# Optimization experiments

Hardware: AMD Instinct MI355X
Metric: run time of the kernel (lower is better)

## Reference

```python
import jax, jax.numpy as jnp
import numpy as np

# dims
A, T, K, H, NH, F, L = 64, 50, 6, 128, 8, 60, 512
M = A * T * K          # 19200 mode nodes (layout: agent, time, mode)
AT = A * T             # 3200 agent-timestep nodes
NL = 10                # GA layers: t2m,l2m,m2m_h,m2m_a,m2m_s,t2n,l2n,n2n_h,n2n_a,n2n_s
FF = 4 * H
E = 150000


def _ln(x, g, b):
    mu = x.mean(-1, keepdims=True)
    var = jnp.mean((x - mu) ** 2, axis=-1, keepdims=True)
    return (x - mu) * jax.lax.rsqrt(var + 1e-5) * g + b


def _mlp(x, W1, b1, W2, b2):
    return jax.nn.relu(x @ W1 + b1) @ W2 + b2


def _edge_emb(attr, i, eW1, eb1, eW2, eb2):
    # pad raw edge features to width 5 so all embed MLPs share a stacked param layout
    x = jnp.pad(attr, ((0, 0), (0, 5 - attr.shape[-1])))
    return jax.nn.relu(x @ eW1[i] + eb1[i]) @ eW2[i] + eb2[i]


def _segment_softmax(scores, dst, n):
    smax = jax.ops.segment_max(scores, dst, num_segments=n)
    smax = jnp.where(jnp.isfinite(smax), smax, 0.0)
    ex = jnp.exp(scores - smax[dst])
    den = jax.ops.segment_sum(ex, dst, num_segments=n)
    return ex / (den[dst] + 1e-9)


def _graph_attention(i, x_src, x_dst, ei, edge_emb, p):
    (Wq, Wk, Wv, Wo, Wke, Wve, g1, b1, g2, b2, fW1, fb1, fW2, fb2) = p
    src, dst = ei[0], ei[1]
    dh = H // NH
    n_dst = x_dst.shape[0]
    xd = _ln(x_dst, g1[i], b1[i])
    xs = _ln(x_src, g1[i], b1[i])
    q = (xd @ Wq[i]).reshape(n_dst, NH, dh)
    k = (xs @ Wk[i])[src]            # gather per-edge keys  [E,H]
    v = (xs @ Wv[i])[src]
    if edge_emb is not None:
        k = k + edge_emb @ Wke[i]
        v = v + edge_emb @ Wve[i]
    k = k.reshape(-1, NH, dh)
    v = v.reshape(-1, NH, dh)
    scores = jnp.sum(q[dst] * k, axis=-1) / np.sqrt(dh)   # [E,NH]
    attn = _segment_softmax(scores, dst, n_dst)
    agg = jax.ops.segment_sum(attn[..., None] * v, dst, num_segments=n_dst)
    x = x_dst + agg.reshape(n_dst, H) @ Wo[i]
    h = _ln(x, g2[i], b2[i])
    return x + _mlp(h, fW1[i], fb1[i], fW2[i], fb2[i])


def _forward(a_input, l_embs, mode_tokens,
             emb_W1, emb_b1, emb_W2, emb_b2,
             ga_Wq, ga_Wk, ga_Wv, ga_Wo, ga_Wke, ga_Wve,
             ga_g1, ga_b1, ga_g2, ga_b2, ga_fW1, ga_fb1, ga_fW2, ga_fb2,
             tp_W1, tp_b1, tp_W2, tp_b2,
             pa_W1, pa_b1, pa_W2, pa_b2,
             tr_W1, tr_b1, tr_W2, tr_b2,
             t2m_attr, l2m_attr, m2m_h_attr, m2m_a_attr,
             t2m_ei, l2m_ei, m2m_h_ei, m2m_a_ei, m2m_s_ei):
    ga = (ga_Wq, ga_Wk, ga_Wv, ga_Wo, ga_Wke, ga_Wve,
          ga_g1, ga_b1, ga_g2, ga_b2, ga_fW1, ga_fb1, ga_fW2, ga_fb2)
    # agent embedding: TwoLayerMLP on [vel_len, vel_theta, length, width, type]
    a_embs = (jax.nn.relu(a_input @ emb_W1[0] + emb_b1[0]) @ emb_W2[0] + emb_b2[0]).reshape(AT, H)
    # mode tokens broadcast over (agent, time)
    m = jnp.broadcast_to(mode_tokens, (A, T, K, H)).reshape(M, H)
    # edge-attr embeddings (gather-compute pattern)
    t2m_e = _edge_emb(t2m_attr, 1, emb_W1, emb_b1, emb_W2, emb_b2)
    l2m_e = _edge_emb(l2m_attr, 2, emb_W1, emb_b1, emb_W2, emb_b2)
    m2m_h_e = _edge_emb(m2m_h_attr, 3, emb_W1, emb_b1, emb_W2, emb_b2)
    m2m_a_e = _edge_emb(m2m_a_attr, 4, emb_W1, emb_b1, emb_W2, emb_b2)
    # proposal stage
    m = _graph_attention(0, a_embs, m, t2m_ei, t2m_e, ga)
    m = _graph_attention(1, l_embs, m, l2m_ei, l2m_e, ga)
    m = _graph_attention(2, m, m, m2m_h_ei, m2m_h_e, ga)
    m = _graph_attention(3, m, m, m2m_a_ei, m2m_a_e, ga)
    m = _graph_attention(4, m, m, m2m_s_ei, None, ga)
    m_last = m.reshape(A, T, K, H)[:, -1]                 # [A,K,H]
    proposal = _mlp(m_last, tp_W1, tp_b1, tp_W2, tp_b2)   # [A,K,2F]
    anchor = _mlp(proposal, pa_W1, pa_b1, pa_W2, pa_b2)   # [A,K,H]
    # refinement stage on anchor-conditioned mode nodes
    n = (m.reshape(A, T, K, H) + anchor[:, None]).reshape(M, H)
    n = _graph_attention(5, a_embs, n, t2m_ei, t2m_e, ga)
    n = _graph_attention(6, l_embs, n, l2m_ei, l2m_e, ga)
    n = _graph_attention(7, n, n, m2m_h_ei, m2m_h_e, ga)
    n = _graph_attention(8, n, n, m2m_a_ei, m2m_a_e, ga)
    n = _graph_attention(9, n, n, m2m_s_ei, None, ga)
    n_last = n.reshape(A, T, K, H)[:, -1]
    refine = proposal + _mlp(n_last, tr_W1, tr_b1, tr_W2, tr_b2)
    return jnp.stack([proposal, refine])                  # [2,A,K,2F]


def setup_inputs() -> dict:
    key = jax.random.key(0)
    ks = list(jax.random.split(key, 64))
    it = iter(ks)
    nx = lambda: next(it)
    p = lambda *s: 0.02 * jax.random.normal(nx(), s, dtype=jnp.float32)
    inp = {}
    inp['a_input'] = jax.random.normal(nx(), (A, T, 5), dtype=jnp.float32)
    inp['l_embs'] = jax.random.normal(nx(), (L, H), dtype=jnp.float32)
    inp['mode_tokens'] = p(K, H)
    # stacked edge/feature embed MLPs: 0:a,1:t2m,2:l2m,3:m2m_h,4:m2m_a
    inp['emb_W1'] = p(5, 5, H); inp['emb_b1'] = jnp.zeros((5, H), jnp.float32)
    inp['emb_W2'] = p(5, H, H); inp['emb_b2'] = jnp.zeros((5, H), jnp.float32)
    # stacked GraphAttention params
    for nm in ['ga_Wq', 'ga_Wk', 'ga_Wv', 'ga_Wo', 'ga_Wke', 'ga_Wve']:
        inp[nm] = p(NL, H, H)
    inp['ga_g1'] = jnp.ones((NL, H), jnp.float32); inp['ga_b1'] = jnp.zeros((NL, H), jnp.float32)
    inp['ga_g2'] = jnp.ones((NL, H), jnp.float32); inp['ga_b2'] = jnp.zeros((NL, H), jnp.float32)
    inp['ga_fW1'] = p(NL, H, FF); inp['ga_fb1'] = jnp.zeros((NL, FF), jnp.float32)
    inp['ga_fW2'] = p(NL, FF, H); inp['ga_fb2'] = jnp.zeros((NL, H), jnp.float32)
    # heads
    inp['tp_W1'] = p(H, H); inp['tp_b1'] = jnp.zeros((H,), jnp.float32)
    inp['tp_W2'] = p(H, 2 * F); inp['tp_b2'] = jnp.zeros((2 * F,), jnp.float32)
    inp['pa_W1'] = p(2 * F, H); inp['pa_b1'] = jnp.zeros((H,), jnp.float32)
    inp['pa_W2'] = p(H, H); inp['pa_b2'] = jnp.zeros((H,), jnp.float32)
    inp['tr_W1'] = p(H, H); inp['tr_b1'] = jnp.zeros((H,), jnp.float32)
    inp['tr_W2'] = p(H, 2 * F); inp['tr_b2'] = jnp.zeros((2 * F,), jnp.float32)
    # raw edge features
    inp['t2m_attr'] = jax.random.normal(nx(), (E, 4), dtype=jnp.float32)
    inp['l2m_attr'] = jax.random.normal(nx(), (E, 3), dtype=jnp.float32)
    inp['m2m_h_attr'] = jax.random.normal(nx(), (E, 4), dtype=jnp.float32)
    inp['m2m_a_attr'] = jax.random.normal(nx(), (E, 3), dtype=jnp.float32)
    # edge indices (src row range differs per graph)
    ri = lambda hi: jax.random.randint(nx(), (E,), 0, hi, dtype=jnp.int32)
    inp['t2m_ei'] = jnp.stack([ri(AT), ri(M)])
    inp['l2m_ei'] = jnp.stack([ri(L), ri(M)])
    inp['m2m_h_ei'] = jnp.stack([ri(M), ri(M)])
    inp['m2m_a_ei'] = jnp.stack([ri(M), ri(M)])
    inp['m2m_s_ei'] = jnp.stack([ri(M), ri(M)])
    return inp


def reference(a_input, l_embs, mode_tokens,
              emb_W1, emb_b1, emb_W2, emb_b2,
              ga_Wq, ga_Wk, ga_Wv, ga_Wo, ga_Wke, ga_Wve,
              ga_g1, ga_b1, ga_g2, ga_b2, ga_fW1, ga_fb1, ga_fW2, ga_fb2,
              tp_W1, tp_b1, tp_W2, tp_b2,
              pa_W1, pa_b1, pa_W2, pa_b2,
              tr_W1, tr_b1, tr_W2, tr_b2,
              t2m_attr, l2m_attr, m2m_h_attr, m2m_a_attr,
              t2m_ei, l2m_ei, m2m_h_ei, m2m_a_ei, m2m_s_ei):
    return _forward(a_input, l_embs, mode_tokens,
                    emb_W1, emb_b1, emb_W2, emb_b2,
                    ga_Wq, ga_Wk, ga_Wv, ga_Wo, ga_Wke, ga_Wve,
                    ga_g1, ga_b1, ga_g2, ga_b2, ga_fW1, ga_fb1, ga_fW2, ga_fb2,
                    tp_W1, tp_b1, tp_W2, tp_b2,
                    pa_W1, pa_b1, pa_W2, pa_b2,
                    tr_W1, tr_b1, tr_W2, tr_b2,
                    t2m_attr, l2m_attr, m2m_h_attr, m2m_a_attr,
                    t2m_ei, l2m_ei, m2m_h_ei, m2m_a_ei, m2m_s_ei)
```

## Files before the change

### kernel.cpp

```cpp
#include <hip/hip_runtime.h>
#include <hip/hip_bf16.h>
#include <math.h>

#define DEV __device__ __forceinline__

typedef __attribute__((ext_vector_type(4))) float floatx4;
typedef __attribute__((ext_vector_type(8))) __bf16 bf16x8;

static constexpr int A_ = 64, T_ = 50, K_ = 6, H_ = 128, NH_ = 8, F_ = 60, L_ = 512;
static constexpr int M_  = A_ * T_ * K_;
static constexpr int AT_ = A_ * T_;
static constexpr int FF_ = 4 * H_;
static constexpr int NL_ = 10;
static constexpr int P2F = 2 * F_;
static constexpr int AK_ = A_ * K_;
static constexpr size_t WLAY = 196608;
static constexpr int NB_ = (M_ + 255) / 256;

DEV ushort f2bh(float f) {
    unsigned u = __float_as_uint(f);
    unsigned r = u + 0x7FFFu + ((u >> 16) & 1u);
    return (ushort)(r >> 16);
}
DEV float bh2f(ushort h) { return __uint_as_float(((unsigned)h) << 16); }

__global__ __launch_bounds__(256) void ln_stats(const float* __restrict__ x,
                                                float* __restrict__ mu,
                                                float* __restrict__ rs, int n) {
    int row = blockIdx.x * 4 + (threadIdx.x >> 6);
    int lane = threadIdx.x & 63;
    if (row >= n) return;
    const float* xr = x + (size_t)row * H_;
    float v0 = xr[lane], v1 = xr[lane + 64];
    float s = v0 + v1;
    for (int m = 32; m >= 1; m >>= 1) s += __shfl_xor(s, m, 64);
    float m_ = s * (1.f / 128.f);
    float d0 = v0 - m_, d1 = v1 - m_;
    float vs = d0 * d0 + d1 * d1;
    for (int m = 32; m >= 1; m >>= 1) vs += __shfl_xor(vs, m, 64);
    if (lane == 0) {
        mu[row] = m_;
        rs[row] = rsqrtf(vs * (1.f / 128.f) + 1e-5f);
    }
}

template <int ACT, bool RES, int OMODE, bool LNX>
__global__ __launch_bounds__(256) void mgemm(const float* __restrict__ X,
                                             const ushort* __restrict__ Wh,
                                             const ushort* __restrict__ Wl,
                                             const float* __restrict__ bias,
                                             const float* __restrict__ res,
                                             float* __restrict__ Y,
                                             ushort* __restrict__ Yb,
                                             const float* __restrict__ muv,
                                             const float* __restrict__ rsv,
                                             const float* __restrict__ lng,
                                             const float* __restrict__ lnb,
                                             int n, int Kd, int C) {
    __shared__ ushort lds[4 * 8192];
    ushort* Xh  = lds;
    ushort* Xl  = lds + 8192;
    ushort* Wsh = lds + 16384;
    ushort* Wsl = lds + 24576;
    int row0 = blockIdx.x * 128, col0 = blockIdx.y * 128;
    int tid = threadIdx.x;
    int lane = tid & 63, wid = tid >> 6;
    int rbase = (wid >> 1) * 64, cbase = (wid & 1) * 64;
    int lrow = lane & 15, lk = lane >> 4;
    floatx4 acc[4][4];
#pragma unroll
    for (int a = 0; a < 4; a++)
#pragma unroll
        for (int b2 = 0; b2 < 4; b2++) acc[a][b2] = floatx4{0.f, 0.f, 0.f, 0.f};

    for (int k0 = 0; k0 < Kd; k0 += 64) {
        float4 g4, b4;
        if (LNX) {
            int kcol = k0 + (tid & 15) * 4;
            g4 = *(const float4*)(lng + kcol);
            b4 = *(const float4*)(lnb + kcol);
        }
#pragma unroll
        for (int i = 0; i < 8; i++) {
            int idx = tid + i * 256;
            int r = idx >> 4, kc = idx & 15;
            float4 v = *(const float4*)(X + (size_t)(row0 + r) * Kd + k0 + kc * 4);
            if (LNX) {
                float mur = muv[row0 + r];
                float rsr = rsv[row0 + r];
                v.x = (v.x - mur) * rsr * g4.x + b4.x;
                v.y = (v.y - mur) * rsr * g4.y + b4.y;
                v.z = (v.z - mur) * rsr * g4.z + b4.z;
                v.w = (v.w - mur) * rsr * g4.w + b4.w;
            }
            ushort h0 = f2bh(v.x), h1 = f2bh(v.y), h2 = f2bh(v.z), h3 = f2bh(v.w);
            ushort l0 = f2bh(v.x - bh2f(h0)), l1 = f2bh(v.y - bh2f(h1)),
                   l2 = f2bh(v.z - bh2f(h2)), l3 = f2bh(v.w - bh2f(h3));
            int base = (r << 6) + (((kc >> 1) ^ (r & 7)) << 3) + ((kc & 1) << 2);
            *(ushort4*)(Xh + base) = make_ushort4(h0, h1, h2, h3);
            *(ushort4*)(Xl + base) = make_ushort4(l0, l1, l2, l3);
        }
#pragma unroll
        for (int i = 0; i < 4; i++) {
            int idx = tid + i * 256;
            int c = idx >> 3, ch = idx & 7;
            int base = (c << 6) + ((ch ^ (c & 7)) << 3);
            size_t go = (size_t)(col0 + c) * Kd + k0 + ch * 8;
            *(float4*)(Wsh + base) = *(const float4*)(Wh + go);
            *(float4*)(Wsl + base) = *(const float4*)(Wl + go);
        }
        __syncthreads();
#pragma unroll
        for (int kk = 0; kk < 2; kk++) {
            int ch = kk * 4 + lk;
            bf16x8 xh[4], xl[4], wh[4], wl[4];
#pragma unroll
            for (int s = 0; s < 4; s++) {
                int r = rbase + s * 16 + lrow;
                int xoff = (r << 6) + ((ch ^ (r & 7)) << 3);
                xh[s] = *(const bf16x8*)(Xh + xoff);
                xl[s] = *(const bf16x8*)(Xl + xoff);
                int c = cbase + s * 16 + lrow;
                int woff = (c << 6) + ((ch ^ (c & 7)) << 3);
                wh[s] = *(const bf16x8*)(Wsh + woff);
                wl[s] = *(const bf16x8*)(Wsl + woff);
            }
#pragma unroll
            for (int sr = 0; sr < 4; sr++)
#pragma unroll
                for (int sc = 0; sc < 4; sc++) {
                    acc[sr][sc] = __builtin_amdgcn_mfma_f32_16x16x32_bf16(wh[sc], xh[sr], acc[sr][sc], 0, 0, 0);
                    acc[sr][sc] = __builtin_amdgcn_mfma_f32_16x16x32_bf16(wl[sc], xh[sr], acc[sr][sc], 0, 0, 0);
                    acc[sr][sc] = __builtin_amdgcn_mfma_f32_16x16x32_bf16(wh[sc], xl[sr], acc[sr][sc], 0, 0, 0);
                }
        }
        __syncthreads();
    }
#pragma unroll
    for (int sr = 0; sr < 4; sr++) {
        int row = row0 + rbase + sr * 16 + lrow;
#pragma unroll
        for (int sc = 0; sc < 4; sc++) {
            int col = col0 + cbase + sc * 16 + lk * 4;
            float4 v = make_float4(acc[sr][sc][0], acc[sr][sc][1],
                                   acc[sr][sc][2], acc[sr][sc][3]);
            if (bias) { float4 bv = *(const float4*)(bias + col);
                        v.x += bv.x; v.y += bv.y; v.z += bv.z; v.w += bv.w; }
            if (ACT == 1) { v.x = fmaxf(v.x, 0.f); v.y = fmaxf(v.y, 0.f);
                            v.z = fmaxf(v.z, 0.f); v.w = fmaxf(v.w, 0.f); }
            if (OMODE == 0) {
                size_t o = (size_t)row * C + col;
                if (RES) { float4 rv = *(const float4*)(res + o);
                           v.x += rv.x; v.y += rv.y; v.z += rv.z; v.w += rv.w; }
                *(float4*)(Y + o) = v;
            } else if (OMODE == 1) {
                size_t o = (size_t)row * C + col;
                *(ushort4*)(Yb + o) = make_ushort4(f2bh(v.x), f2bh(v.y), f2bh(v.z), f2bh(v.w));
            } else {
                if (col0 == 0) {
                    *(float4*)(Y + (size_t)row * 128 + col) = v;
                } else {
                    *(ushort4*)(Yb + (size_t)row * 256 + (col - 128)) =
                        make_ushort4(f2bh(v.x), f2bh(v.y), f2bh(v.z), f2bh(v.w));
                }
            }
        }
    }
}

__global__ __launch_bounds__(256) void prep_w(const float* __restrict__ Wq,
                                              const float* __restrict__ Wk,
                                              const float* __restrict__ Wv,
                                              const float* __restrict__ Wo,
                                              const float* __restrict__ fW1,
                                              const float* __restrict__ fW2,
                                              ushort* __restrict__ oh,
                                              ushort* __restrict__ ol) {
    int l = blockIdx.y, t = blockIdx.x;
    const float* src; int K, C, tiles_c; size_t obase;
    if (t < 64) {
        int mi = t >> 4; t &= 15;
        src = (mi == 0 ? Wq : mi == 1 ? Wk : mi == 2 ? Wv : Wo) + (size_t)l * 16384;
        K = 128; C = 128; tiles_c = 4; obase = (size_t)l * WLAY + (size_t)mi * 16384;
    } else if (t < 128) {
        t -= 64; src = fW1 + (size_t)l * 65536;
        K = 128; C = 512; tiles_c = 16; obase = (size_t)l * WLAY + 65536;
    } else {
        t -= 128; src = fW2 + (size_t)l * 65536;
        K = 512; C = 128; tiles_c = 4; obase = (size_t)l * WLAY + 131072;
    }
    int tc = t % tiles_c, tk = t / tiles_c;
    __shared__ float tile[32][33];
    int tx = threadIdx.x & 31, ty = threadIdx.x >> 5;
#pragma unroll
    for (int i = 0; i < 4; i++) {
        int k = tk * 32 + ty + i * 8;
        tile[ty + i * 8][tx] = src[(size_t)k * C + tc * 32 + tx];
    }
    __syncthreads();
#pragma unroll
    for (int i = 0; i < 4; i++) {
        int c = tc * 32 + ty + i * 8;
        float v = tile[tx][ty + i * 8];
        ushort h = f2bh(v);
        ushort lo = f2bh(v - bh2f(h));
        size_t o = obase + (size_t)c * K + tk * 32 + tx;
        oh[o] = h; ol[o] = lo;
    }
}

template <int ACT, bool RES>
__global__ void small_gemm(const float* __restrict__ X, const float* __restrict__ W,
                           const float* __restrict__ bias, const float* __restrict__ res,
                           float* __restrict__ Y, int n, int Kd, int C) {
    int idx = blockIdx.x * 256 + threadIdx.x;
    if (idx >= n * C) return;
    int row = idx / C, c = idx - row * C;
    float a = bias ? bias[c] : 0.f;
    const float* xr = X + (size_t)row * Kd;
    for (int k = 0; k < Kd; k++) a = fmaf(xr[k], W[(size_t)k * C + c], a);
    if (ACT == 1) a = fmaxf(a, 0.f);
    if (RES) a += res[idx];
    Y[idx] = a;
}

__global__ __launch_bounds__(256) void combine_fast(const float* __restrict__ eW2,
                                                    const float* __restrict__ Wke,
                                                    const float* __restrict__ Wve,
                                                    float* __restrict__ cW) {
    __shared__ float Xs[128 * 36];
    __shared__ float Ws[32 * 128];
    int x = blockIdx.x;
    int li = x & 7, kv = x >> 3;
    int l = li < 4 ? li : li + 1;
    int g = (li & 3) + 1;
    const float* E2 = eW2 + (size_t)g * 16384;
    const float* Wp = (kv ? Wve : Wke) + (size_t)l * 16384;
    float* out = cW + (size_t)l * 32768 + kv * 128;
    int tid = threadIdx.x;
    int tc = tid & 15, tr = tid >> 4;
    int cA = tc * 4, rA = tr * 4;
    float acc[8][8] = {};
    for (int j0 = 0; j0 < 128; j0 += 32) {
#pragma unroll
        for (int i = 0; i < 4; i++) {
            int idx = tid + i * 256;
            int r = idx >> 3, jc = idx & 7;
            *(float4*)(Xs + r * 36 + jc * 4) =
                *(const float4*)(E2 + (size_t)r * 128 + j0 + jc * 4);
        }
#pragma unroll
        for (int i = 0; i < 4; i++) {
            int idx = tid + i * 256;
            int cc = idx & 31, jj = idx >> 5;
            *(float4*)(Ws + jj * 128 + cc * 4) =
                *(const float4*)(Wp + (size_t)(j0 + jj) * 128 + cc * 4);
        }
        __syncthreads();
#pragma unroll 8
        for (int jj = 0; jj < 32; jj++) {
            float4 w0 = *(const float4*)(Ws + jj * 128 + cA);
            float4 w1 = *(const float4*)(Ws + jj * 128 + cA + 64);
            float xr[8];
#pragma unroll
            for (int i2 = 0; i2 < 4; i2++) {
                xr[i2]     = Xs[(rA + i2) * 36 + jj];
                xr[4 + i2] = Xs[(rA + i2 + 64) * 36 + jj];
            }
#pragma unroll
            for (int i2 = 0; i2 < 8; i2++) {
                float xv = xr[i2];
                acc[i2][0] = fmaf(xv, w0.x, acc[i2][0]);
                acc[i2][1] = fmaf(xv, w0.y, acc[i2][1]);
                acc[i2][2] = fmaf(xv, w0.z, acc[i2][2]);
                acc[i2][3] = fmaf(xv, w0.w, acc[i2][3]);
                acc[i2][4] = fmaf(xv, w1.x, acc[i2][4]);
                acc[i2][5] = fmaf(xv, w1.y, acc[i2][5]);
                acc[i2][6] = fmaf(xv, w1.z, acc[i2][6]);
                acc[i2][7] = fmaf(xv, w1.w, acc[i2][7]);
            }
        }
        __syncthreads();
    }
#pragma unroll
    for (int i = 0; i < 8; i++) {
        int r = (i < 4) ? (rA + i) : (rA + i + 60);
#pragma unroll
        for (int chh = 0; chh < 2; chh++) {
            int c = cA + chh * 64;
            *(float4*)(out + (size_t)r * 256 + c) =
                make_float4(acc[i][chh * 4 + 0], acc[i][chh * 4 + 1],
                            acc[i][chh * 4 + 2], acc[i][chh * 4 + 3]);
        }
    }
}
__global__ void combine_bias(const float* __restrict__ eb2,
                             const float* __restrict__ Wke,
                             const float* __restrict__ Wve,
                             float* __restrict__ cb) {
    int x = blockIdx.x;
    int li = x & 7, kv = x >> 3;
    int l = li < 4 ? li : li + 1;
    int g = (li & 3) + 1;
    const float* Wp = (kv ? Wve : Wke) + (size_t)l * 16384;
    const float* eb = eb2 + g * 128;
    int cc = threadIdx.x;
    float a = 0.f;
    for (int j = 0; j < 128; j++) a = fmaf(eb[j], Wp[(size_t)j * 128 + cc], a);
    cb[l * 256 + kv * 128 + cc] = a;
}

__global__ void zero_i32(int* __restrict__ p, int n) {
    int i = blockIdx.x * 256 + threadIdx.x;
    if (i < n) p[i] = 0;
}
__global__ void hist_kernel(const int* __restrict__ dst, int E, int* __restrict__ deg) {
    int e = blockIdx.x * 256 + threadIdx.x;
    if (e < E) atomicAdd(&deg[dst[e]], 1);
}
__global__ __launch_bounds__(256) void exscan5(const int* __restrict__ deg0,
                                               int* __restrict__ off0,
                                               int* __restrict__ cursor0, int n) {
    int g = blockIdx.x;
    const int* deg = deg0 + (size_t)g * n;
    int* off = off0 + (size_t)g * (n + 1);
    int* cursor = cursor0 + (size_t)g * n;
    __shared__ int wsum[4];
    __shared__ int carry;
    int tid = threadIdx.x, lane = tid & 63, w = tid >> 6;
    if (tid == 0) carry = 0;
    __syncthreads();
    for (int base = 0; base < n; base += 256) {
        int v = (base + tid < n) ? deg[base + tid] : 0;
        int incl = v;
        for (int d = 1; d < 64; d <<= 1) {
            int t = __shfl_up(incl, d, 64);
            if (lane >= d) incl += t;
        }
        if (lane == 63) wsum[w] = incl;
        __syncthreads();
        int woff = 0;
        for (int i = 0; i < w; i++) woff += wsum[i];
        int total = wsum[0] + wsum[1] + wsum[2] + wsum[3];
        int excl = carry + woff + incl - v;
        if (base + tid < n) { off[base + tid] = excl; cursor[base + tid] = excl; }
        __syncthreads();
        if (tid == 0) carry += total;
        __syncthreads();
    }
    if (threadIdx.x == 0) off[n] = carry;
}
__global__ void scatter_kernel(const int* __restrict__ dst, int E,
                               int* __restrict__ cursor, int* __restrict__ eids) {
    int e = blockIdx.x * 256 + threadIdx.x;
    if (e < E) { int p = atomicAdd(&cursor[dst[e]], 1); eids[p] = e; }
}
__global__ void sort_edges(const int* __restrict__ eid, const int* __restrict__ srcArr,
                           const float* __restrict__ attr, int aw, int E,
                           int* __restrict__ esrc, float4* __restrict__ eattr) {
    int pos = blockIdx.x * 256 + threadIdx.x;
    if (pos >= E) return;
    int e = eid[pos];
    esrc[pos] = srcArr[e];
    if (attr) {
        float4 v;
        v.x = attr[(size_t)e * aw + 0];
        v.y = attr[(size_t)e * aw + 1];
        v.z = (aw > 2) ? attr[(size_t)e * aw + 2] : 0.f;
        v.w = (aw > 3) ? attr[(size_t)e * aw + 3] : 0.f;
        eattr[pos] = v;
    }
}

__global__ __launch_bounds__(256) void hist_deg2(const int* __restrict__ deg5, int n,
                                                 int* __restrict__ bh) {
    int g = blockIdx.y;
    const int* deg = deg5 + (size_t)g * n;
    __shared__ int lh[33];
    if (threadIdx.x < 33) lh[threadIdx.x] = 0;
    __syncthreads();
    int d = blockIdx.x * 256 + threadIdx.x;
    if (d < n) { int b = deg[d]; if (b > 32) b = 32; atomicAdd(&lh[b], 1); }
    __syncthreads();
    if (threadIdx.x < 33)
        bh[((size_t)g * NB_ + blockIdx.x) * 33 + threadIdx.x] = lh[threadIdx.x];
}
__global__ __launch_bounds__(64) void scan_bh(int* __restrict__ bh) {
    int g = blockIdx.x;
    int* p = bh + (size_t)g * NB_ * 33;
    __shared__ int tot[33], base[33];
    int bin = threadIdx.x;
    if (bin < 33) {
        int t = 0;
        for (int b = 0; b < NB_; b++) t += p[b * 33 + bin];
        tot[bin] = t;
    }
    __syncthreads();
    if (threadIdx.x == 0) {
        int acc = 0;
        for (int i = 0; i < 33; i++) { base[i] = acc; acc += tot[i]; }
    }
    __syncthreads();
    if (bin < 33) {
        int run = base[bin];
        for (int b = 0; b < NB_; b++) { int v = p[b * 33 + bin]; p[b * 33 + bin] = run; run += v; }
    }
}
__global__ __launch_bounds__(256) void scatter_ord2(const int* __restrict__ deg5, int n,
                                                    const int* __restrict__ bh,
                                                    int* __restrict__ dord5) {
    int g = blockIdx.y;
    const int* deg = deg5 + (size_t)g * n;
    int* dord = dord5 + (size_t)g * n;
    __shared__ int cur[33];
    if (threadIdx.x < 33)
        cur[threadIdx.x] = bh[((size_t)g * NB_ + blockIdx.x) * 33 + threadIdx.x];
    __syncthreads();
    int d = blockIdx.x * 256 + threadIdx.x;
    if (d < n) {
        int b = deg[d]; if (b > 32) b = 32;
        int p = atomicAdd(&cur[b], 1);
        dord[p] = d;
    }
}

__global__ __launch_bounds__(256) void prep_g(const float* __restrict__ q,
                                              const float* __restrict__ cWl,
                                              const float* __restrict__ cbl,
                                              ushort* __restrict__ g,
                                              float* __restrict__ sb) {
    __shared__ float qs[8 * 132];
    int tid = threadIdx.x;
    int cp = tid & 127, hb = (tid >> 7) * 4;
    float ck[64];
    {
        const float* csrc = cWl + (size_t)cp * 256 + hb * 16;
#pragma unroll
        for (int t4 = 0; t4 < 16; t4++) {
            float4 v = *(const float4*)(csrc + t4 * 4);
            ck[t4 * 4 + 0] = v.x; ck[t4 * 4 + 1] = v.y;
            ck[t4 * 4 + 2] = v.z; ck[t4 * 4 + 3] = v.w;
        }
    }
    int d0 = blockIdx.x * 8;
    {
        int dl = tid >> 5, col = (tid & 31) * 4;
        *(float4*)(qs + dl * 132 + col) = *(const float4*)(q + (size_t)(d0 + dl) * 128 + col);
    }
    __syncthreads();
#pragma unroll
    for (int dl = 0; dl < 8; dl++) {
        const float* qr = qs + dl * 132 + hb * 16;
        float a0 = 0.f, a1 = 0.f, a2 = 0.f, a3 = 0.f;
#pragma unroll
        for (int t = 0; t < 16; t++) {
            a0 = fmaf(ck[t],      qr[t],      a0);
            a1 = fmaf(ck[16 + t], qr[16 + t], a1);
            a2 = fmaf(ck[32 + t], qr[32 + t], a2);
            a3 = fmaf(ck[48 + t], qr[48 + t], a3);
        }
        ushort4 o = make_ushort4(f2bh(a0 * 0.25f), f2bh(a1 * 0.25f),
                                 f2bh(a2 * 0.25f), f2bh(a3 * 0.25f));
        *(ushort4*)(g + (size_t)(d0 + dl) * 1024 + cp * 8 + hb) = o;
    }
    if (tid < 64) {
        int dl = tid >> 3, h = tid & 7;
        const float* qr = qs + dl * 132 + h * 16;
        const float* cbr = cbl + h * 16;
        float a = 0.f;
#pragma unroll
        for (int t = 0; t < 16; t++) a = fmaf(cbr[t], qr[t], a);
        sb[(d0 + dl) * 8 + h] = a * 0.25f;
    }
}

__global__ __launch_bounds__(256) void attn_fact(const int* __restrict__ dord,
                                                 const int* __restrict__ off,
                                                 const int* __restrict__ esrc,
                                                 const float4* __restrict__ eattr,
                                                 const ushort* __restrict__ g,
                                                 const float* __restrict__ sb,
                                                 const float* __restrict__ eW1,
                                                 const float* __restrict__ eb1,
                                                 const float* __restrict__ q,
                                                 const ushort* __restrict__ kvp,
                                                 ushort* __restrict__ hsum,
                                                 float* __restrict__ vxacc,
                                                 float* __restrict__ den) {
    __shared__ float lds[4 * 144];
    int w = threadIdx.x >> 6, l = threadIdx.x & 63;
    int i = l & 15, hlo = l >> 4;
    float* hw = lds + w * 144;
    int d = dord[blockIdx.x * 4 + w];
    int beg = off[d], end = off[d + 1];
    float q0 = q[(size_t)d * 128 + l] * 0.25f;
    float q1 = q[(size_t)d * 128 + 64 + l] * 0.25f;
    float gA[8], gB[8];
#pragma unroll
    for (int j = 0; j < 8; j++) {
        gA[j] = bh2f(g[(size_t)d * 1024 + (j * 16 + i) * 8 + hlo]);
        gB[j] = bh2f(g[(size_t)d * 1024 + (j * 16 + i) * 8 + hlo + 4]);
    }
    float sbA = sb[d * 8 + hlo], sbB = sb[d * 8 + 4 + hlo];
    float w1a[4], w1b[4];
#pragma unroll
    for (int j = 0; j < 4; j++) { w1a[j] = eW1[j * 128 + l]; w1b[j] = eW1[j * 128 + 64 + l]; }
    float ebA = eb1[l], ebB = eb1[64 + l];
    float dnA = 0.f, dnB = 0.f;
    float accL[8] = {}, accH[8] = {};
    float va0 = 0.f, va1 = 0.f;
    float4 atA = make_float4(0.f, 0.f, 0.f, 0.f), atB = atA;
    ushort kA0 = 0, kA1 = 0, vA0 = 0, vA1 = 0;
    ushort kB0 = 0, kB1 = 0, vB0 = 0, vB1 = 0;
    auto LOADE = [&](int p, float4& at, ushort& ka, ushort& kb, ushort& va, ushort& vb) {
        int s = esrc[p]; at = eattr[p];
        const ushort* r = kvp + (size_t)s * 256;
        ka = r[l]; kb = r[64 + l];
        va = r[128 + l]; vb = r[192 + l];
    };
    if (beg < end) LOADE(beg, atA, kA0, kA1, vA0, vA1);
    if (beg + 1 < end) LOADE(beg + 1, atB, kB0, kB1, vB0, vB1);
    for (int pos = beg; pos < end; pos++) {
        float4 at = atA;
        ushort rk0 = kA0, rk1 = kA1, rv0 = vA0, rv1 = vA1;
        atA = atB; kA0 = kB0; kA1 = kB1; vA0 = vB0; vA1 = vB1;
        if (pos + 2 < end) LOADE(pos + 2, atB, kB0, kB1, vB0, vB1);
        float h0 = fmaxf(ebA + at.x * w1a[0] + at.y * w1a[1] + at.z * w1a[2] + at.w * w1a[3], 0.f);
        float h1 = fmaxf(ebB + at.x * w1b[0] + at.y * w1b[1] + at.z * w1b[2] + at.w * w1b[3], 0.f);
        hw[l] = h0; hw[64 + l] = h1;
        __builtin_amdgcn_wave_barrier();
        float pA = q0 * bh2f(rk0), pB = q1 * bh2f(rk1);
#pragma unroll
        for (int j = 0; j < 8; j++) {
            float hv = hw[j * 16 + i];
            pA = fmaf(hv, gA[j], pA);
            pB = fmaf(hv, gB[j], pB);
        }
#pragma unroll
        for (int msk = 1; msk < 16; msk <<= 1) {
            pA += __shfl_xor(pA, msk, 64);
            pB += __shfl_xor(pB, msk, 64);
        }
        float wA = __expf(pA + sbA);
        float wB = __expf(pB + sbB);
        dnA += wA; dnB += wB;
        va0 = fmaf(wA, bh2f(rv0), va0);
        va1 = fmaf(wB, bh2f(rv1), va1);
        if (i == 0) { hw[128 + hlo] = wA; hw[132 + hlo] = wB; }
        __builtin_amdgcn_wave_barrier();
        float4 WA = *(float4*)(hw + 128), WB = *(float4*)(hw + 132);
#pragma unroll
        for (int j = 0; j < 4; j++) {
            float wa = ((const float*)&WA)[j];
            float wb = ((const float*)&WB)[j];
            accL[j]     = fmaf(wa, h0, accL[j]);
            accH[j]     = fmaf(wa, h1, accH[j]);
            accL[4 + j] = fmaf(wb, h0, accL[4 + j]);
            accH[4 + j] = fmaf(wb, h1, accH[4 + j]);
        }
    }
#pragma unroll
    for (int h = 0; h < 8; h++) {
        hsum[(size_t)d * 1024 + h * 128 + l]      = f2bh(accL[h]);
        hsum[(size_t)d * 1024 + h * 128 + 64 + l] = f2bh(accH[h]);
    }
    vxacc[(size_t)d * 128 + l] = va0;
    vxacc[(size_t)d * 128 + 64 + l] = va1;
    if (i == 0) { den[d * 8 + hlo] = dnA; den[d * 8 + 4 + hlo] = dnB; }
}

__global__ __launch_bounds__(256) void attn_plain(const int* __restrict__ dord,
                                                  const int* __restrict__ off,
                                                  const int* __restrict__ esrc,
                                                  const float* __restrict__ q,
                                                  const ushort* __restrict__ kvp,
                                                  float* __restrict__ agg) {
    int lane = threadIdx.x & 63;
    int d = dord[blockIdx.x * 4 + (threadIdx.x >> 6)];
    int beg = off[d], end = off[d + 1];
    float q0 = q[(size_t)d * 128 + lane] * 0.25f;
    float q1 = q[(size_t)d * 128 + 64 + lane] * 0.25f;
    float den0 = 0.f, den1 = 0.f, acc0 = 0.f, acc1 = 0.f;
    ushort kA0 = 0, kA1 = 0, vA0 = 0, vA1 = 0;
    ushort kB0 = 0, kB1 = 0, vB0 = 0, vB1 = 0;
    auto LOADE = [&](int p, ushort& ka, ushort& kb, ushort& va, ushort& vb) {
        int s = esrc[p];
        const ushort* r = kvp + (size_t)s * 256;
        ka = r[lane]; kb = r[64 + lane];
        va = r[128 + lane]; vb = r[192 + lane];
    };
    if (beg < end) LOADE(beg, kA0, kA1, vA0, vA1);
    if (beg + 1 < end) LOADE(beg + 1, kB0, kB1, vB0, vB1);
    for (int pos = beg; pos < end; pos++) {
        ushort rk0 = kA0, rk1 = kA1, rv0 = vA0, rv1 = vA1;
        kA0 = kB0; kA1 = kB1; vA0 = vB0; vA1 = vB1;
        if (pos + 2 < end) LOADE(pos + 2, kB0, kB1, vB0, vB1);
        float p0 = q0 * bh2f(rk0), p1 = q1 * bh2f(rk1);
#pragma unroll
        for (int msk = 1; msk < 16; msk <<= 1) {
            p0 += __shfl_xor(p0, msk, 64);
            p1 += __shfl_xor(p1, msk, 64);
        }
        float w0 = __expf(p0), w1 = __expf(p1);
        den0 += w0; den1 += w1;
        acc0 = fmaf(w0, bh2f(rv0), acc0);
        acc1 = fmaf(w1, bh2f(rv1), acc1);
    }
    agg[(size_t)d * 128 + lane]      = acc0 / (den0 + 1e-9f);
    agg[(size_t)d * 128 + 64 + lane] = acc1 / (den1 + 1e-9f);
}

static constexpr int HST_ = 1092;
__global__ __launch_bounds__(256) void agg_fin(const ushort* __restrict__ hsum,
                                               const float* __restrict__ vxacc,
                                               const float* __restrict__ den,
                                               const float* __restrict__ cWl,
                                               const float* __restrict__ cbl,
                                               float* __restrict__ agg) {
    __shared__ float Cvs[128 * 128];
    __shared__ float hstage[8 * HST_];
    __shared__ float dens[64];
    int tid = threadIdx.x;
    {
        int cp = tid >> 1, cb0 = (tid & 1) * 64;
#pragma unroll
        for (int kq = 0; kq < 16; kq++)
            *(float4*)(Cvs + cp * 128 + cb0 + kq * 4) =
                *(const float4*)(cWl + (size_t)cp * 256 + 128 + cb0 + kq * 4);
    }
    int j = tid & 31, dsel = tid >> 5;
    int c4 = j * 4, h = j >> 2;
    float4 cvb = *(const float4*)(cbl + 128 + c4);
    for (int d0 = blockIdx.x * 8; d0 < M_; d0 += gridDim.x * 8) {
        __syncthreads();
        int r = tid * 4;
#pragma unroll
        for (int k = 0; k < 8; k++) {
            ushort4 u = *(const ushort4*)(hsum + (size_t)(d0 + k) * 1024 + r);
            *(float4*)(hstage + k * HST_ + (r >> 7) * 136 + (r & 127)) =
                make_float4(bh2f(u.x), bh2f(u.y), bh2f(u.z), bh2f(u.w));
        }
        if (tid < 64) dens[tid] = den[d0 * 8 + tid];
        __syncthreads();
        int d = d0 + dsel;
        float dn = dens[dsel * 8 + h];
        float inv = 1.f / (dn + 1e-9f);
        float cf = dn * inv;
        float a0 = 0.f, a1 = 0.f, a2 = 0.f, a3 = 0.f;
        const float* hrow = hstage + dsel * HST_ + h * 136;
#pragma unroll 4
        for (int cpp = 0; cpp < 128; cpp++) {
            float hs = hrow[cpp];
            float4 cv = *(float4*)(Cvs + cpp * 128 + c4);
            a0 = fmaf(hs, cv.x, a0); a1 = fmaf(hs, cv.y, a1);
            a2 = fmaf(hs, cv.z, a2); a3 = fmaf(hs, cv.w, a3);
        }
        float4 vv = *(const float4*)(vxacc + (size_t)d * 128 + c4);
        float4 o;
        o.x = (vv.x + a0) * inv + cvb.x * cf;
        o.y = (vv.y + a1) * inv + cvb.y * cf;
        o.z = (vv.z + a2) * inv + cvb.z * cf;
        o.w = (vv.w + a3) * inv + cvb.w * cf;
        *(float4*)(agg + (size_t)d * 128 + c4) = o;
    }
}

__global__ void mode_init(float* __restrict__ m, const float* __restrict__ mt) {
    int idx = blockIdx.x * 256 + threadIdx.x;
    if (idx >= M_ * H_) return;
    int node = idx >> 7, c = idx & 127;
    m[idx] = mt[(node % K_) * H_ + c];
}
__global__ void extract_last(const float* __restrict__ m, float* __restrict__ out) {
    int idx = blockIdx.x * 256 + threadIdx.x;
    if (idx >= AK_ * H_) return;
    int row = idx >> 7, c = idx & 127;
    int a = row / K_, k = row - a * K_;
    int node = (a * T_ + (T_ - 1)) * K_ + k;
    out[idx] = m[(size_t)node * H_ + c];
}
__global__ void add_anchor(float* __restrict__ m, const float* __restrict__ anchor) {
    int idx = blockIdx.x * 256 + threadIdx.x;
    if (idx >= M_ * H_) return;
    int node = idx >> 7, c = idx & 127;
    int a = node / (T_ * K_), k = node % K_;
    m[idx] += anchor[(size_t)(a * K_ + k) * H_ + c];
}

extern "C" void kernel_launch(void* const* d_in, const int* in_sizes, int n_in,
                              void* d_out, int out_size, void* d_ws, size_t ws_size,
                              hipStream_t stream) {
    const float* a_input     = (const float*)d_in[0];
    const float* l_embs      = (const float*)d_in[1];
    const float* mode_tokens = (const float*)d_in[2];
    const float* emb_W1 = (const float*)d_in[3];
    const float* emb_b1 = (const float*)d_in[4];
    const float* emb_W2 = (const float*)d_in[5];
    const float* emb_b2 = (const float*)d_in[6];
    const float* ga_Wq  = (const float*)d_in[7];
    const float* ga_Wk  = (const float*)d_in[8];
    const float* ga_Wv  = (const float*)d_in[9];
    const float* ga_Wo  = (const float*)d_in[10];
    const float* ga_Wke = (const float*)d_in[11];
    const float* ga_Wve = (const float*)d_in[12];
    const float* ga_g1  = (const float*)d_in[13];
    const float* ga_b1  = (const float*)d_in[14];
    const float* ga_g2  = (const float*)d_in[15];
    const float* ga_b2  = (const float*)d_in[16];
    const float* ga_fW1 = (const float*)d_in[17];
    const float* ga_fb1 = (const float*)d_in[18];
    const float* ga_fW2 = (const float*)d_in[19];
    const float* ga_fb2 = (const float*)d_in[20];
    const float* tp_W1 = (const float*)d_in[21];
    const float* tp_b1 = (const float*)d_in[22];
    const float* tp_W2 = (const float*)d_in[23];
    const float* tp_b2 = (const float*)d_in[24];
    const float* pa_W1 = (const float*)d_in[25];
    const float* pa_b1 = (const float*)d_in[26];
    const float* pa_W2 = (const float*)d_in[27];
    const float* pa_b2 = (const float*)d_in[28];
    const float* tr_W1 = (const float*)d_in[29];
    const float* tr_b1 = (const float*)d_in[30];
    const float* tr_W2 = (const float*)d_in[31];
    const float* tr_b2 = (const float*)d_in[32];
    const float* attrs[4] = { (const float*)d_in[33], (const float*)d_in[34],
                              (const float*)d_in[35], (const float*)d_in[36] };
    const int* eis[5] = { (const int*)d_in[37], (const int*)d_in[38], (const int*)d_in[39],
                          (const int*)d_in[40], (const int*)d_in[41] };
    int Es[5];
    int Emax = 0;
    for (int i = 0; i < 5; i++) { Es[i] = in_sizes[37 + i] / 2; if (Es[i] > Emax) Emax = Es[i]; }

    size_t off = 0;
    auto alloc = [&](size_t nbytes) -> char* {
        char* p = (char*)d_ws + off;
        off += ((nbytes + 255) / 256) * 256;
        return p;
    };
    float* cW     = (float*)alloc((size_t)NL_ * 128 * 256 * 4);
    float* cb     = (float*)alloc((size_t)NL_ * 256 * 4);
    ushort* wbh   = (ushort*)alloc((size_t)NL_ * WLAY * 2);
    ushort* wbl   = (ushort*)alloc((size_t)NL_ * WLAY * 2);
    float* a_embs = (float*)alloc((size_t)AT_ * H_ * 4);
    float* m      = (float*)alloc((size_t)M_ * H_ * 4);
    float* q      = (float*)alloc((size_t)M_ * H_ * 4);
    ushort* kvb   = (ushort*)alloc((size_t)M_ * 256 * 2);
    float* agg    = (float*)alloc((size_t)M_ * H_ * 4);
    float* big    = (float*)alloc((size_t)M_ * FF_ * 4);
    ushort* gbuf  = (ushort*)alloc((size_t)M_ * 1024 * 2);
    ushort* hsumb = (ushort*)alloc((size_t)M_ * 1024 * 2);
    float* vxacc  = (float*)alloc((size_t)M_ * H_ * 4);
    float* den    = (float*)alloc((size_t)M_ * 8 * 4);
    float* sb     = (float*)alloc((size_t)M_ * 8 * 4);
    float* muM    = (float*)alloc((size_t)M_ * 4);
    float* rsM    = (float*)alloc((size_t)M_ * 4);
    float* muA    = (float*)alloc((size_t)AT_ * 4);
    float* rsA    = (float*)alloc((size_t)AT_ * 4);
    float* muL    = (float*)alloc((size_t)L_ * 4);
    float* rsL    = (float*)alloc((size_t)L_ * 4);
    int* csr_off  = (int*)alloc((size_t)5 * (M_ + 1) * 4);
    int* csr_eid  = (int*)alloc((size_t)5 * Emax * 4);
    int* esrc     = (int*)alloc((size_t)5 * Emax * 4);
    float4* eattr = (float4*)alloc((size_t)4 * Emax * 16);
    int* deg5     = (int*)alloc((size_t)5 * M_ * 4);
    int* cursor5  = (int*)alloc((size_t)5 * M_ * 4);
    int* dord5    = (int*)alloc((size_t)5 * M_ * 4);
    int* bh5      = (int*)alloc((size_t)5 * NB_ * 33 * 4);
    float* mlast  = (float*)alloc((size_t)AK_ * H_ * 4);
    float* hbuf   = (float*)alloc((size_t)AK_ * H_ * 4);
    float* anchor = (float*)alloc((size_t)AK_ * H_ * 4);
    (void)ws_size; (void)n_in;

    float* outp = (float*)d_out;

    zero_i32<<<(5 * M_ + 255) / 256, 256, 0, stream>>>(deg5, 5 * M_);
    for (int gI = 0; gI < 5; gI++)
        hist_kernel<<<(Es[gI] + 255) / 256, 256, 0, stream>>>(eis[gI] + Es[gI], Es[gI], deg5 + (size_t)gI * M_);
    exscan5<<<5, 256, 0, stream>>>(deg5, csr_off, cursor5, M_);
    for (int gI = 0; gI < 5; gI++)
        scatter_kernel<<<(Es[gI] + 255) / 256, 256, 0, stream>>>(eis[gI] + Es[gI], Es[gI],
            cursor5 + (size_t)gI * M_, csr_eid + (size_t)gI * Emax);
    for (int gI = 0; gI < 5; gI++) {
        int aw = (gI == 0 || gI == 2) ? 4 : (gI == 4 ? 0 : 3);
        sort_edges<<<(Es[gI] + 255) / 256, 256, 0, stream>>>(
            csr_eid + (size_t)gI * Emax, eis[gI], (gI < 4) ? attrs[gI] : nullptr, aw, Es[gI],
            esrc + (size_t)gI * Emax, eattr + (size_t)gI * Emax);
    }
    hist_deg2<<<dim3(NB_, 5), 256, 0, stream>>>(deg5, M_, bh5);
    scan_bh<<<5, 64, 0, stream>>>(bh5);
    scatter_ord2<<<dim3(NB_, 5), 256, 0, stream>>>(deg5, M_, bh5, dord5);

    prep_w<<<dim3(192, 10), 256, 0, stream>>>(ga_Wq, ga_Wk, ga_Wv, ga_Wo, ga_fW1, ga_fW2, wbh, wbl);
    combine_fast<<<16, 256, 0, stream>>>(emb_W2, ga_Wke, ga_Wve, cW);
    combine_bias<<<16, 128, 0, stream>>>(emb_b2, ga_Wke, ga_Wve, cb);

    small_gemm<1, false><<<(AT_ * H_ + 255) / 256, 256, 0, stream>>>(a_input, emb_W1, emb_b1, nullptr, big, AT_, 5, H_);
    small_gemm<0, false><<<(AT_ * H_ + 255) / 256, 256, 0, stream>>>(big, emb_W2, emb_b2, nullptr, a_embs, AT_, H_, H_);
    mode_init<<<(M_ * H_ + 255) / 256, 256, 0, stream>>>(m, mode_tokens);
    ln_stats<<<AT_ / 4, 256, 0, stream>>>(a_embs, muA, rsA, AT_);
    ln_stats<<<L_ / 4, 256, 0, stream>>>(l_embs, muL, rsL, L_);

    struct Cfg { const float* srcX; const float* muS; const float* rsS; int n_src; int gi; bool hasE; };
    Cfg cfgs[10] = {
        { a_embs, muA, rsA, AT_, 0, true }, { l_embs, muL, rsL, L_, 1, true },
        { nullptr, nullptr, nullptr, M_, 2, true }, { nullptr, nullptr, nullptr, M_, 3, true },
        { nullptr, nullptr, nullptr, M_, 4, false },
        { a_embs, muA, rsA, AT_, 0, true }, { l_embs, muL, rsL, L_, 1, true },
        { nullptr, nullptr, nullptr, M_, 2, true }, { nullptr, nullptr, nullptr, M_, 3, true },
        { nullptr, nullptr, nullptr, M_, 4, false },
    };

    for (int l = 0; l < 10; l++) {
        const Cfg& cf = cfgs[l];
        const int* offg = csr_off + cf.gi * (M_ + 1);
        const int* esrcg = esrc + (size_t)cf.gi * Emax;
        const float4* eattrg = eattr + (size_t)cf.gi * Emax;
        const int* dordg = dord5 + (size_t)cf.gi * M_;
        const float* g1 = ga_g1 + l * H_; const float* b1 = ga_b1 + l * H_;
        size_t wb = (size_t)l * WLAY;

        ln_stats<<<M_ / 4, 256, 0, stream>>>(m, muM, rsM, M_);
        if (cf.srcX) {
            mgemm<0, false, 0, true><<<dim3(M_ / 128, 1), 256, 0, stream>>>(
                m, wbh + wb, wbl + wb, nullptr, nullptr, q, nullptr,
                muM, rsM, g1, b1, M_, 128, 128);
            mgemm<0, false, 1, true><<<dim3(cf.n_src / 128, 2), 256, 0, stream>>>(
                cf.srcX, wbh + wb + 16384, wbl + wb + 16384, nullptr, nullptr, nullptr, kvb,
                cf.muS, cf.rsS, g1, b1, cf.n_src, 128, 256);
        } else {
            mgemm<0, false, 2, true><<<dim3(M_ / 128, 3), 256, 0, stream>>>(
                m, wbh + wb, wbl + wb, nullptr, nullptr, q, kvb,
                muM, rsM, g1, b1, M_, 128, 384);
        }

        if (cf.hasE) {
            int gg = (l < 5) ? l + 1 : l - 4;
            const float* eW1g = emb_W1 + (size_t)gg * 5 * H_;
            const float* eb1g = emb_b1 + (size_t)gg * H_;
            prep_g<<<M_ / 8, 256, 0, stream>>>(q, cW + (size_t)l * 128 * 256, cb + l * 256, gbuf, sb);
            attn_fact<<<M_ / 4, 256, 0, stream>>>(dordg, offg, esrcg, eattrg, gbuf, sb, eW1g, eb1g,
                                                  q, kvb, hsumb, vxacc, den);
            agg_fin<<<256, 256, 0, stream>>>(hsumb, vxacc, den,
                                             cW + (size_t)l * 128 * 256, cb + l * 256, agg);
        } else {
            attn_plain<<<M_ / 4, 256, 0, stream>>>(dordg, offg, esrcg, q, kvb, agg);
        }

        mgemm<0, true, 0, false><<<dim3(M_ / 128, 1), 256, 0, stream>>>(
            agg, wbh + wb + 49152, wbl + wb + 49152, nullptr, m, m, nullptr,
            nullptr, nullptr, nullptr, nullptr, M_, 128, 128);
        ln_stats<<<M_ / 4, 256, 0, stream>>>(m, muM, rsM, M_);
        mgemm<1, false, 0, true><<<dim3(M_ / 128, 4), 256, 0, stream>>>(
            m, wbh + wb + 65536, wbl + wb + 65536, ga_fb1 + l * FF_, nullptr, big, nullptr,
            muM, rsM, ga_g2 + l * H_, ga_b2 + l * H_, M_, 128, 512);
        mgemm<0, true, 0, false><<<dim3(M_ / 128, 1), 256, 0, stream>>>(
            big, wbh + wb + 131072, wbl + wb + 131072, ga_fb2 + l * H_, m, m, nullptr,
            nullptr, nullptr, nullptr, nullptr, M_, 512, 128);

        if (l == 4) {
            extract_last<<<(AK_ * H_ + 255) / 256, 256, 0, stream>>>(m, mlast);
            small_gemm<1, false><<<(AK_ * H_ + 255) / 256, 256, 0, stream>>>(mlast, tp_W1, tp_b1, nullptr, hbuf, AK_, H_, H_);
            small_gemm<0, false><<<(AK_ * P2F + 255) / 256, 256, 0, stream>>>(hbuf, tp_W2, tp_b2, nullptr, outp, AK_, H_, P2F);
            small_gemm<1, false><<<(AK_ * H_ + 255) / 256, 256, 0, stream>>>(outp, pa_W1, pa_b1, nullptr, hbuf, AK_, P2F, H_);
            small_gemm<0, false><<<(AK_ * H_ + 255) / 256, 256, 0, stream>>>(hbuf, pa_W2, pa_b2, nullptr, anchor, AK_, H_, H_);
            add_anchor<<<(M_ * H_ + 255) / 256, 256, 0, stream>>>(m, anchor);
        }
    }

    extract_last<<<(AK_ * H_ + 255) / 256, 256, 0, stream>>>(m, mlast);
    small_gemm<1, false><<<(AK_ * H_ + 255) / 256, 256, 0, stream>>>(mlast, tr_W1, tr_b1, nullptr, hbuf, AK_, H_, H_);
    small_gemm<0, true><<<(AK_ * P2F + 255) / 256, 256, 0, stream>>>(hbuf, tr_W2, tr_b2, outp, outp + AK_ * P2F, AK_, H_, P2F);
}
```

Baseline: 2.654 ms.

## Fuse LayerNorm stats into residual GEMM epilogues and merge agg_fin into attn_fact

The residual-output GEMMs now compute per-row sum and sum of squares in their epilogue and write mean and rstd directly. This removes the standalone ln_stats passes before each attention block and before the FFN; ln_stats still runs at init and after the anchor add. The agg_fin kernel is folded into attn_fact, which stages per-destination results in shared memory and applies the value projection in-block. That avoids writing and rereading the bf16 hsum, vxacc and den buffers. The trade-offs are a one-pass variance formula (E[x²]−μ²) that is less numerically stable, and a per-block fp32 matvec that reads cW from global memory instead of shared memory.

```diff
diff --git a/kernel.cpp b/kernel.cpp
--- a/kernel.cpp
+++ b/kernel.cpp
@@ -44,7 +44,7 @@
     }
 }
 
-template <int ACT, bool RES, int OMODE, bool LNX>
+template <int ACT, bool RES, int OMODE, bool LNX, bool STATS>
 __global__ __launch_bounds__(256) void mgemm(const float* __restrict__ X,
                                              const ushort* __restrict__ Wh,
                                              const ushort* __restrict__ Wl,
@@ -56,6 +56,8 @@
                                              const float* __restrict__ rsv,
                                              const float* __restrict__ lng,
                                              const float* __restrict__ lnb,
+                                             float* __restrict__ muo,
+                                             float* __restrict__ rso,
                                              int n, int Kd, int C) {
     __shared__ ushort lds[4 * 8192];
     ushort* Xh  = lds;
@@ -136,6 +138,7 @@
         }
         __syncthreads();
     }
+    float rowsum[4] = {}, rowsq[4] = {};
 #pragma unroll
     for (int sr = 0; sr < 4; sr++) {
         int row = row0 + rbase + sr * 16 + lrow;
@@ -152,6 +155,10 @@
                 size_t o = (size_t)row * C + col;
                 if (RES) { float4 rv = *(const float4*)(res + o);
                            v.x += rv.x; v.y += rv.y; v.z += rv.z; v.w += rv.w; }
+                if (STATS) {
+                    rowsum[sr] += v.x + v.y + v.z + v.w;
+                    rowsq[sr]  += v.x * v.x + v.y * v.y + v.z * v.z + v.w * v.w;
+                }
                 *(float4*)(Y + o) = v;
             } else if (OMODE == 1) {
                 size_t o = (size_t)row * C + col;
@@ -164,6 +171,27 @@
                         make_ushort4(f2bh(v.x), f2bh(v.y), f2bh(v.z), f2bh(v.w));
                 }
             }
+        }
+    }
+    if (STATS) {
+        float* sums = (float*)lds;
+        float* sqs  = ((float*)lds) + 1024;
+        int slot = (wid & 1) * 4 + lk;
+#pragma unroll
+        for (int sr = 0; sr < 4; sr++) {
+            int rl = rbase + sr * 16 + lrow;
+            sums[rl * 8 + slot] = rowsum[sr];
+            sqs[rl * 8 + slot]  = rowsq[sr];
+        }
+        __syncthreads();
+        if (tid < 128) {
+            float s = 0.f, sq = 0.f;
+#pragma unroll
+            for (int t = 0; t < 8; t++) { s += sums[tid * 8 + t]; sq += sqs[tid * 8 + t]; }
+            float mu = s * (1.f / 128.f);
+            float var = sq * (1.f / 128.f) - mu * mu;
+            muo[row0 + tid] = mu;
+            rso[row0 + tid] = rsqrtf(var + 1e-5f);
         }
     }
 }
@@ -484,13 +512,17 @@
                                                  const float* __restrict__ eb1,
                                                  const float* __restrict__ q,
                                                  const ushort* __restrict__ kvp,
-                                                 ushort* __restrict__ hsum,
-                                                 float* __restrict__ vxacc,
-                                                 float* __restrict__ den) {
-    __shared__ float lds[4 * 144];
+                                                 const float* __restrict__ cWl,
+                                                 const float* __restrict__ cbl,
+                                                 float* __restrict__ agg) {
+    __shared__ float hw4[4 * 144];
+    __shared__ float hstage[4][1024];
+    __shared__ float vstage[4][128];
+    __shared__ float dens2[4][8];
+    __shared__ int sD[4];
     int w = threadIdx.x >> 6, l = threadIdx.x & 63;
     int i = l & 15, hlo = l >> 4;
-    float* hw = lds + w * 144;
+    float* hw = hw4 + w * 144;
     int d = dord[blockIdx.x * 4 + w];
     int beg = off[d], end = off[d + 1];
     float q0 = q[(size_t)d * 128 + l] * 0.25f;
@@ -561,12 +593,35 @@
     }
 #pragma unroll
     for (int h = 0; h < 8; h++) {
-        hsum[(size_t)d * 1024 + h * 128 + l]      = f2bh(accL[h]);
-        hsum[(size_t)d * 1024 + h * 128 + 64 + l] = f2bh(accH[h]);
-    }
-    vxacc[(size_t)d * 128 + l] = va0;
-    vxacc[(size_t)d * 128 + 64 + l] = va1;
-    if (i == 0) { den[d * 8 + hlo] = dnA; den[d * 8 + 4 + hlo] = dnB; }
+        hstage[w][h * 128 + l]      = accL[h];
+        hstage[w][h * 128 + 64 + l] = accH[h];
+    }
+    vstage[w][l] = va0; vstage[w][64 + l] = va1;
+    if (i == 0) { dens2[w][hlo] = dnA; dens2[w][4 + hlo] = dnB; }
+    if (l == 0) sD[w] = d;
+    __syncthreads();
+    {
+        int cc = threadIdx.x & 127, grp = threadIdx.x >> 7;
+        int ds0 = grp * 2, ds1 = grp * 2 + 1;
+        int hh = cc >> 4;
+        float dn0 = dens2[ds0][hh], dn1 = dens2[ds1][hh];
+        float inv0 = 1.f / (dn0 + 1e-9f), cf0 = dn0 * inv0;
+        float inv1 = 1.f / (dn1 + 1e-9f), cf1 = dn1 * inv1;
+        const float* hr0 = &hstage[ds0][hh * 128];
+        const float* hr1 = &hstage[ds1][hh * 128];
+        const float* cvp = cWl + 128 + cc;
+        float a0 = 0.f, a1 = 0.f;
+#pragma unroll 4
+        for (int cp = 0; cp < 128; cp++) {
+            float cv = cvp[(size_t)cp * 256];
+            a0 = fmaf(hr0[cp], cv, a0);
+            a1 = fmaf(hr1[cp], cv, a1);
+        }
+        float cvb = cbl[128 + cc];
+        int dd0 = sD[ds0], dd1 = sD[ds1];
+        agg[(size_t)dd0 * 128 + cc] = (vstage[ds0][cc] + a0) * inv0 + cvb * cf0;
+        agg[(size_t)dd1 * 128 + cc] = (vstage[ds1][cc] + a1) * inv1 + cvb * cf1;
+    }
 }
 
 __global__ __launch_bounds__(256) void attn_plain(const int* __restrict__ dord,
@@ -608,61 +663,6 @@
     }
     agg[(size_t)d * 128 + lane]      = acc0 / (den0 + 1e-9f);
     agg[(size_t)d * 128 + 64 + lane] = acc1 / (den1 + 1e-9f);
-}
-
-static constexpr int HST_ = 1092;
-__global__ __launch_bounds__(256) void agg_fin(const ushort* __restrict__ hsum,
-                                               const float* __restrict__ vxacc,
-                                               const float* __restrict__ den,
-                                               const float* __restrict__ cWl,
-                                               const float* __restrict__ cbl,
-                                               float* __restrict__ agg) {
-    __shared__ float Cvs[128 * 128];
-    __shared__ float hstage[8 * HST_];
-    __shared__ float dens[64];
-    int tid = threadIdx.x;
-    {
-        int cp = tid >> 1, cb0 = (tid & 1) * 64;
-#pragma unroll
-        for (int kq = 0; kq < 16; kq++)
-            *(float4*)(Cvs + cp * 128 + cb0 + kq * 4) =
-                *(const float4*)(cWl + (size_t)cp * 256 + 128 + cb0 + kq * 4);
-    }
-    int j = tid & 31, dsel = tid >> 5;
-    int c4 = j * 4, h = j >> 2;
-    float4 cvb = *(const float4*)(cbl + 128 + c4);
-    for (int d0 = blockIdx.x * 8; d0 < M_; d0 += gridDim.x * 8) {
-        __syncthreads();
-        int r = tid * 4;
-#pragma unroll
-        for (int k = 0; k < 8; k++) {
-            ushort4 u = *(const ushort4*)(hsum + (size_t)(d0 + k) * 1024 + r);
-            *(float4*)(hstage + k * HST_ + (r >> 7) * 136 + (r & 127)) =
-                make_float4(bh2f(u.x), bh2f(u.y), bh2f(u.z), bh2f(u.w));
-        }
-        if (tid < 64) dens[tid] = den[d0 * 8 + tid];
-        __syncthreads();
-        int d = d0 + dsel;
-        float dn = dens[dsel * 8 + h];
-        float inv = 1.f / (dn + 1e-9f);
-        float cf = dn * inv;
-        float a0 = 0.f, a1 = 0.f, a2 = 0.f, a3 = 0.f;
-        const float* hrow = hstage + dsel * HST_ + h * 136;
-#pragma unroll 4
-        for (int cpp = 0; cpp < 128; cpp++) {
-            float hs = hrow[cpp];
-            float4 cv = *(float4*)(Cvs + cpp * 128 + c4);
-            a0 = fmaf(hs, cv.x, a0); a1 = fmaf(hs, cv.y, a1);
-            a2 = fmaf(hs, cv.z, a2); a3 = fmaf(hs, cv.w, a3);
-        }
-        float4 vv = *(const float4*)(vxacc + (size_t)d * 128 + c4);
-        float4 o;
-        o.x = (vv.x + a0) * inv + cvb.x * cf;
-        o.y = (vv.y + a1) * inv + cvb.y * cf;
-        o.z = (vv.z + a2) * inv + cvb.z * cf;
-        o.w = (vv.w + a3) * inv + cvb.w * cf;
-        *(float4*)(agg + (size_t)d * 128 + c4) = o;
-    }
 }
 
 __global__ void mode_init(float* __restrict__ m, const float* __restrict__ mt) {
@@ -748,9 +748,6 @@
     float* agg    = (float*)alloc((size_t)M_ * H_ * 4);
     float* big    = (float*)alloc((size_t)M_ * FF_ * 4);
     ushort* gbuf  = (ushort*)alloc((size_t)M_ * 1024 * 2);
-    ushort* hsumb = (ushort*)alloc((size_t)M_ * 1024 * 2);
-    float* vxacc  = (float*)alloc((size_t)M_ * H_ * 4);
-    float* den    = (float*)alloc((size_t)M_ * 8 * 4);
     float* sb     = (float*)alloc((size_t)M_ * 8 * 4);
     float* muM    = (float*)alloc((size_t)M_ * 4);
     float* rsM    = (float*)alloc((size_t)M_ * 4);
@@ -797,6 +794,7 @@
     small_gemm<1, false><<<(AT_ * H_ + 255) / 256, 256, 0, stream>>>(a_input, emb_W1, emb_b1, nullptr, big, AT_, 5, H_);
     small_gemm<0, false><<<(AT_ * H_ + 255) / 256, 256, 0, stream>>>(big, emb_W2, emb_b2, nullptr, a_embs, AT_, H_, H_);
     mode_init<<<(M_ * H_ + 255) / 256, 256, 0, stream>>>(m, mode_tokens);
+    ln_stats<<<M_ / 4, 256, 0, stream>>>(m, muM, rsM, M_);
     ln_stats<<<AT_ / 4, 256, 0, stream>>>(a_embs, muA, rsA, AT_);
     ln_stats<<<L_ / 4, 256, 0, stream>>>(l_embs, muL, rsL, L_);
 
@@ -819,43 +817,39 @@
         const float* g1 = ga_g1 + l * H_; const float* b1 = ga_b1 + l * H_;
         size_t wb = (size_t)l * WLAY;
 
-        ln_stats<<<M_ / 4, 256, 0, stream>>>(m, muM, rsM, M_);
         if (cf.srcX) {
-            mgemm<0, false, 0, true><<<dim3(M_ / 128, 1), 256, 0, stream>>>(
+            mgemm<0, false, 0, true, false><<<dim3(M_ / 128, 1), 256, 0, stream>>>(
                 m, wbh + wb, wbl + wb, nullptr, nullptr, q, nullptr,
-                muM, rsM, g1, b1, M_, 128, 128);
-            mgemm<0, false, 1, true><<<dim3(cf.n_src / 128, 2), 256, 0, stream>>>(
+                muM, rsM, g1, b1, nullptr, nullptr, M_, 128, 128);
+            mgemm<0, false, 1, true, false><<<dim3(cf.n_src / 128, 2), 256, 0, stream>>>(
                 cf.srcX, wbh + wb + 16384, wbl + wb + 16384, nullptr, nullptr, nullptr, kvb,
-                cf.muS, cf.rsS, g1, b1, cf.n_src, 128, 256);
+                cf.muS, cf.rsS, g1, b1, nullptr, nullptr, cf.n_src, 128, 256);
         } else {
-            mgemm<0, false, 2, true><<<dim3(M_ / 128, 3), 256, 0, stream>>>(
+            mgemm<0, false, 2, true, false><<<dim3(M_ / 128, 3), 256, 0, stream>>>(
                 m, wbh + wb, wbl + wb, nullptr, nullptr, q, kvb,
-                muM, rsM, g1, b1, M_, 128, 384);
+                muM, rsM, g1, b1, nullptr, nullptr, M_, 128, 384);
         }
 
         if (cf.hasE) {
             int gg = (l < 5) ? l + 1 : l - 4;
             const float* eW1g = emb_W1 + (size_t)gg * 5 * H_;
             const float* eb1g = emb_b1 + (size_t)gg * H_;
-            prep_g<<<M_ / 8, 256, 0, stream>>>(q, cW + (size_t)l * 128 * 256, cb + l * 256, gbuf, sb);
+            prep_g<<<M_ / 8, 256, 0, stream>>>(q, cW + (size_t)l * 32768, cb + l * 256, gbuf, sb);
             attn_fact<<<M_ / 4, 256, 0, stream>>>(dordg, offg, esrcg, eattrg, gbuf, sb, eW1g, eb1g,
-                                                  q, kvb, hsumb, vxacc, den);
-            agg_fin<<<256, 256, 0, stream>>>(hsumb, vxacc, den,
-                                             cW + (size_t)l * 128 * 256, cb + l * 256, agg);
+                                                  q, kvb, cW + (size_t)l * 32768, cb + l * 256, agg);
         } else {
             attn_plain<<<M_ / 4, 256, 0, stream>>>(dordg, offg, esrcg, q, kvb, agg);
         }
 
-        mgemm<0, true, 0, false><<<dim3(M_ / 128, 1), 256, 0, stream>>>(
+        mgemm<0, true, 0, false, true><<<dim3(M_ / 128, 1), 256, 0, stream>>>(
             agg, wbh + wb + 49152, wbl + wb + 49152, nullptr, m, m, nullptr,
-            nullptr, nullptr, nullptr, nullptr, M_, 128, 128);
-        ln_stats<<<M_ / 4, 256, 0, stream>>>(m, muM, rsM, M_);
-        mgemm<1, false, 0, true><<<dim3(M_ / 128, 4), 256, 0, stream>>>(
+            nullptr, nullptr, nullptr, nullptr, muM, rsM, M_, 128, 128);
+        mgemm<1, false, 0, true, false><<<dim3(M_ / 128, 4), 256, 0, stream>>>(
             m, wbh + wb + 65536, wbl + wb + 65536, ga_fb1 + l * FF_, nullptr, big, nullptr,
-            muM, rsM, ga_g2 + l * H_, ga_b2 + l * H_, M_, 128, 512);
-        mgemm<0, true, 0, false><<<dim3(M_ / 128, 1), 256, 0, stream>>>(
+            muM, rsM, ga_g2 + l * H_, ga_b2 + l * H_, nullptr, nullptr, M_, 128, 512);
+        mgemm<0, true, 0, false, true><<<dim3(M_ / 128, 1), 256, 0, stream>>>(
             big, wbh + wb + 131072, wbl + wb + 131072, ga_fb2 + l * H_, m, m, nullptr,
-            nullptr, nullptr, nullptr, nullptr, M_, 512, 128);
+            nullptr, nullptr, nullptr, nullptr, muM, rsM, M_, 512, 128);
 
         if (l == 4) {
             extract_last<<<(AK_ * H_ + 255) / 256, 256, 0, stream>>>(m, mlast);
@@ -864,6 +858,7 @@
             small_gemm<1, false><<<(AK_ * H_ + 255) / 256, 256, 0, stream>>>(outp, pa_W1, pa_b1, nullptr, hbuf, AK_, P2F, H_);
             small_gemm<0, false><<<(AK_ * H_ + 255) / 256, 256, 0, stream>>>(hbuf, pa_W2, pa_b2, nullptr, anchor, AK_, H_, H_);
             add_anchor<<<(M_ * H_ + 255) / 256, 256, 0, stream>>>(m, anchor);
+            ln_stats<<<M_ / 4, 256, 0, stream>>>(m, muM, rsM, M_);
         }
     }
 
```

New measurement: 2.515 ms. -5.2%, faster.
